# Optimization experiments

Hardware: AMD Instinct MI355X
Metric: run time of the kernel (lower is better)

Reference implementation:

```python
import jax, jax.numpy as jnp
import numpy as np

DECAY = 0.8
EPS = 1e-5
COMMIT = 1.0


def setup_inputs() -> dict:
    key = jax.random.key(0)
    k1, k2 = jax.random.split(key)
    x = jax.random.normal(k1, (8, 2048, 512), dtype=jnp.float32)
    embed = jax.random.normal(k2, (4, 2048, 128), dtype=jnp.float32)  # [G, C, dg]
    cluster_size = jnp.zeros((4, 2048), dtype=jnp.float32)            # [G, C]
    embed_avg = embed                                                 # clone of embed, as in torch init
    return {"x": x, "embed": embed, "cluster_size": cluster_size, "embed_avg": embed_avg}


def reference(x, embed, cluster_size, embed_avg):
    B, S, D = x.shape
    G, C, dg = embed.shape
    N = B * S
    # split channels into G groups: [G, N, dg]
    f = x.reshape(N, G, dg).transpose(1, 0, 2)
    # negative squared euclidean distance: -(||f||^2 - 2 f E^T + ||E||^2) -> [G, N, C]
    dist = -(jnp.sum(f * f, axis=-1, keepdims=True)
             - 2.0 * jnp.einsum('gnd,gcd->gnc', f, embed)
             + jnp.sum(embed * embed, axis=-1)[:, None, :])
    ind = jnp.argmax(dist, axis=-1)  # [G, N]
    # gather codes: quantize[g, n] = embed[g, ind[g, n]]
    q = jax.vmap(lambda e_g, i_g: e_g[i_g])(embed, ind)  # [G, N, dg]
    quantize = q.transpose(1, 0, 2).reshape(B, S, D)

    # --- EMA codebook update (training path; buffer updates, no grad in torch) ---
    bins = jax.vmap(lambda i_g: jnp.zeros((C,), x.dtype).at[i_g].add(1.0))(ind)  # [G, C]
    embed_sum = jax.vmap(lambda f_g, i_g: jax.ops.segment_sum(f_g, i_g, num_segments=C))(f, ind)  # [G, C, dg]
    new_cluster_size = cluster_size * DECAY + (1.0 - DECAY) * bins
    new_embed_avg = embed_avg * DECAY + (1.0 - DECAY) * embed_sum
    total = jnp.sum(new_cluster_size, axis=-1, keepdims=True)
    smoothed = (new_cluster_size + EPS) / (total + C * EPS) * total  # laplace smoothing
    new_embed = new_embed_avg / smoothed[..., None]

    # straight-through estimator + commitment loss (VectorQuantize wrapper)
    commit_loss = COMMIT * jnp.mean((jax.lax.stop_gradient(quantize) - x) ** 2)
    quantize_st = x + jax.lax.stop_gradient(quantize - x)
    ind_out = ind.transpose(1, 0).reshape(B, S, G)
    return (quantize_st, ind_out, commit_loss,
            jax.lax.stop_gradient(new_cluster_size),
            jax.lax.stop_gradient(new_embed_avg),
            jax.lax.stop_gradient(new_embed))
```

## Files before the change

### kernel.cpp

```cpp
#include <hip/hip_runtime.h>

#define Bn 8
#define Sn 2048
#define Dn 512
#define Gn 4
#define Cn 2048
#define DGn 128
#define Nn 16384

#define OFF_Q    0u
#define OFF_IND  8388608u
#define OFF_LOSS 8454144u
#define OFF_CS   8454145u
#define OFF_AVG  8462337u
#define OFF_EMB  9510913u

__global__ void vq_init(const float* __restrict__ cs_in,
                        const float* __restrict__ avg_in,
                        float* __restrict__ out) {
    int i = blockIdx.x * 256 + threadIdx.x;
    if (i < Gn * Cn * DGn) out[OFF_AVG + i] = 0.8f * avg_in[i];
    if (i < Gn * Cn)       out[OFF_CS + i]  = 0.8f * cs_in[i];
    if (i == 0)            out[OFF_LOSS] = 0.0f;
}

__global__ void vq_enorm(const float* __restrict__ embed,
                         float* __restrict__ out) {
    int gid  = blockIdx.x * 256 + threadIdx.x;
    int wave = gid >> 6;
    int lane = gid & 63;
    const float* row = embed + (size_t)wave * DGn;
    float a = row[lane], b = row[lane + 64];
    float v = fmaf(a, a, b * b);
    #pragma unroll
    for (int off = 32; off; off >>= 1) v += __shfl_xor(v, off, 64);
    if (lane == 0) out[OFF_EMB + wave] = v;
}

__launch_bounds__(512, 2)
__global__ void vq_main(const float* __restrict__ x,
                        const float* __restrict__ embed,
                        float* __restrict__ out) {
    __shared__ float As[DGn][128];
    __shared__ float Es[8][256];

    const int t  = threadIdx.x;
    const int g  = blockIdx.x >> 7;
    const int n0 = (blockIdx.x & 127) * 128;
    const int tr = t & 15;
    const int tc = t >> 4;

    const float* xg = x + (size_t)n0 * Dn + g * DGn;
    const float* eg = embed + (size_t)g * Cn * DGn;
    const float* enorm_g = out + OFF_EMB + g * Cn;

    {
        const int arow = t & 127, ah = t >> 7;
        const float* xrow = xg + (size_t)arow * Dn;
        #pragma unroll
        for (int j = 0; j < 8; ++j) {
            int q4 = ah + 4 * j;
            float4 v = *(const float4*)(xrow + q4 * 4);
            int k = q4 * 4;
            As[k+0][arow] = v.x; As[k+1][arow] = v.y; As[k+2][arow] = v.z; As[k+3][arow] = v.w;
        }
    }

    float bestv[8];
    int   besti[8];
    #pragma unroll
    for (int i = 0; i < 8; ++i) { bestv[i] = -3.4e38f; besti[i] = 0; }

    const int m0 = 4 * tr;
    const int cb = 4 * tc;
    const int ec = t & 255;
    const int kq = (t >> 8) * 4;

    for (int c0 = 0; c0 < Cn; c0 += 256) {
        float acc[8][8];
        #pragma unroll
        for (int i = 0; i < 8; ++i)
            #pragma unroll
            for (int j = 0; j < 8; ++j) acc[i][j] = 0.f;

        for (int k0 = 0; k0 < DGn; k0 += 8) {
            __syncthreads();
            {
                const float* erow = eg + (size_t)(c0 + ec) * DGn + k0 + kq;
                float4 e0 = *(const float4*)(erow);
                Es[kq+0][ec] = e0.x; Es[kq+1][ec] = e0.y; Es[kq+2][ec] = e0.z; Es[kq+3][ec] = e0.w;
            }
            __syncthreads();
            #pragma unroll
            for (int kk = 0; kk < 8; ++kk) {
                float4 a0 = *(const float4*)&As[k0+kk][m0];
                float4 a1 = *(const float4*)&As[k0+kk][64 + m0];
                float4 b0 = *(const float4*)&Es[kk][cb];
                float4 b1 = *(const float4*)&Es[kk][128 + cb];
                float av[8] = {a0.x,a0.y,a0.z,a0.w,a1.x,a1.y,a1.z,a1.w};
                float bv[8] = {b0.x,b0.y,b0.z,b0.w,b1.x,b1.y,b1.z,b1.w};
                #pragma unroll
                for (int i = 0; i < 8; ++i) {
                    float a = av[i];
                    #pragma unroll
                    for (int j = 0; j < 8; ++j)
                        acc[i][j] = fmaf(a, bv[j], acc[i][j]);
                }
            }
        }
        #pragma unroll
        for (int h = 0; h < 2; ++h) {
            #pragma unroll
            for (int jj = 0; jj < 4; ++jj) {
                int c = c0 + 128*h + cb + jj;
                float en = enorm_g[c];
                #pragma unroll
                for (int i = 0; i < 8; ++i) {
                    float di = fmaf(2.0f, acc[i][4*h + jj], -en);
                    if (di > bestv[i]) { bestv[i] = di; besti[i] = c; }
                }
            }
        }
    }

    float* redv = &As[0][0];
    int*   redi = ((int*)&As[0][0]) + 4352;
    int*   idxf = (int*)&Es[0][0];
    __syncthreads();
    #pragma unroll
    for (int i = 0; i < 8; ++i) {
        int m = (i < 4) ? (m0 + i) : (64 + m0 + i - 4);
        redv[m*33 + tc] = bestv[i];
        redi[m*33 + tc] = besti[i];
    }
    __syncthreads();
    if (t < 128) {
        float bv = redv[t*33]; int bi = redi[t*33];
        #pragma unroll
        for (int u = 1; u < 32; ++u) {
            float v2 = redv[t*33 + u]; int i2 = redi[t*33 + u];
            if (v2 > bv || (v2 == bv && i2 < bi)) { bv = v2; bi = i2; }
        }
        idxf[t] = bi;
        out[OFF_IND + (size_t)(n0 + t) * Gn + g] = (float)bi;
        atomicAdd(&out[OFF_CS + g*Cn + bi], 0.2f);
    }
    __syncthreads();

    float lloss = 0.f;
    for (int j = 0; j < 32; ++j) {
        int e = j * 512 + t;
        int row = e >> 7, d = e & 127;
        int ci = idxf[row];
        float xv = xg[(size_t)row * Dn + d];
        float q  = eg[(size_t)ci * DGn + d];
        out[OFF_Q + (size_t)(n0+row) * Dn + g*DGn + d] = xv + (q - xv);
        atomicAdd(&out[OFF_AVG + ((size_t)g*Cn + ci)*DGn + d], 0.2f * xv);
        float df = q - xv;
        lloss += df * df;
    }
    #pragma unroll
    for (int off = 32; off; off >>= 1) lloss += __shfl_xor(lloss, off, 64);
    if ((t & 63) == 0) atomicAdd(&out[OFF_LOSS], lloss);
}

__global__ void vq_finalize(float* __restrict__ out) {
    const int g = blockIdx.x >> 5;
    const int slice = blockIdx.x & 31;
    const int t = threadIdx.x;
    __shared__ float red[256];
    const float* ncs = out + OFF_CS + g * Cn;
    float s = 0.f;
    for (int c = t; c < Cn; c += 256) s += ncs[c];
    red[t] = s;
    __syncthreads();
    for (int w = 128; w; w >>= 1) {
        if (t < w) red[t] += red[t + w];
        __syncthreads();
    }
    float total = red[0];
    float denom = total + Cn * 1e-5f;
    const float* avg = out + OFF_AVG + (size_t)g * Cn * DGn;
    float* embo = out + OFF_EMB + (size_t)g * Cn * DGn;
    for (int u = 0; u < 32; ++u) {
        int e = slice * 8192 + u * 256 + t;
        int c = e >> 7;
        float sm = (ncs[c] + 1e-5f) / denom * total;
        embo[e] = avg[e] / sm;
    }
    if (blockIdx.x == 0 && t == 0) out[OFF_LOSS] *= (1.0f / 8388608.0f);
}

extern "C" void kernel_launch(void* const* d_in, const int* in_sizes, int n_in,
                              void* d_out, int out_size, void* d_ws, size_t ws_size,
                              hipStream_t stream) {
    const float* x    = (const float*)d_in[0];
    const float* emb  = (const float*)d_in[1];
    const float* cs   = (const float*)d_in[2];
    const float* eavg = (const float*)d_in[3];
    float* out = (float*)d_out;

    hipLaunchKernelGGL(vq_init,     dim3(4096), dim3(256), 0, stream, cs, eavg, out);
    hipLaunchKernelGGL(vq_enorm,    dim3(2048), dim3(256), 0, stream, emb, out);
    hipLaunchKernelGGL(vq_main,     dim3(512),  dim3(512), 0, stream, x, emb, out);
    hipLaunchKernelGGL(vq_finalize, dim3(128),  dim3(256), 0, stream, out);
}
```

Baseline: 535.5 us.

## Double-buffer codebook tiles with register prefetch and widen per-thread tile to 8x16

Restructures the distance GEMM loop so that codebook tiles are 16 deep by 512 codes wide and double-buffered in LDS. The next tile is prefetched into registers while the current one is computed, which cuts the barrier count to one per step. Each thread now accumulates an 8x16 block instead of 8x8, raising arithmetic intensity per LDS load. The cost is roughly double the accumulator registers and a drop to one block per CU in the launch bounds, so occupancy falls and there is a risk of spilling.

Measured after the change: 873.9 us. 63.2% more time.

```diff
diff --git a/kernel.cpp b/kernel.cpp
--- a/kernel.cpp
+++ b/kernel.cpp
@@ -37,12 +37,12 @@
     if (lane == 0) out[OFF_EMB + wave] = v;
 }
 
-__launch_bounds__(512, 2)
+__launch_bounds__(512, 1)
 __global__ void vq_main(const float* __restrict__ x,
                         const float* __restrict__ embed,
                         float* __restrict__ out) {
     __shared__ float As[DGn][128];
-    __shared__ float Es[8][256];
+    __shared__ float Es[2][16][512];
 
     const int t  = threadIdx.x;
     const int g  = blockIdx.x >> 7;
@@ -65,6 +65,18 @@
             As[k+0][arow] = v.x; As[k+1][arow] = v.y; As[k+2][arow] = v.z; As[k+3][arow] = v.w;
         }
     }
+    {
+        const float* er = eg + (size_t)t * DGn;
+        float4 p0 = *(const float4*)(er);
+        float4 p1 = *(const float4*)(er + 4);
+        float4 p2 = *(const float4*)(er + 8);
+        float4 p3 = *(const float4*)(er + 12);
+        Es[0][ 0][t] = p0.x; Es[0][ 1][t] = p0.y; Es[0][ 2][t] = p0.z; Es[0][ 3][t] = p0.w;
+        Es[0][ 4][t] = p1.x; Es[0][ 5][t] = p1.y; Es[0][ 6][t] = p1.z; Es[0][ 7][t] = p1.w;
+        Es[0][ 8][t] = p2.x; Es[0][ 9][t] = p2.y; Es[0][10][t] = p2.z; Es[0][11][t] = p2.w;
+        Es[0][12][t] = p3.x; Es[0][13][t] = p3.y; Es[0][14][t] = p3.z; Es[0][15][t] = p3.w;
+    }
+    __syncthreads();
 
     float bestv[8];
     int   besti[8];
@@ -73,60 +85,83 @@
 
     const int m0 = 4 * tr;
     const int cb = 4 * tc;
-    const int ec = t & 255;
-    const int kq = (t >> 8) * 4;
-
-    for (int c0 = 0; c0 < Cn; c0 += 256) {
-        float acc[8][8];
-        #pragma unroll
-        for (int i = 0; i < 8; ++i)
+
+    float acc[8][16];
+    #pragma unroll
+    for (int i = 0; i < 8; ++i)
+        #pragma unroll
+        for (int j = 0; j < 16; ++j) acc[i][j] = 0.f;
+
+    for (int s = 0; s < 32; ++s) {
+        const int cur = s & 1;
+        const int c0 = (s >> 3) << 9;
+        const int k0 = (s & 7) << 4;
+
+        float4 p0, p1, p2, p3;
+        if (s < 31) {
+            const int s1 = s + 1;
+            const int nc0 = (s1 >> 3) << 9;
+            const int nk0 = (s1 & 7) << 4;
+            const float* er = eg + (size_t)(nc0 + t) * DGn + nk0;
+            p0 = *(const float4*)(er);
+            p1 = *(const float4*)(er + 4);
+            p2 = *(const float4*)(er + 8);
+            p3 = *(const float4*)(er + 12);
+        }
+
+        #pragma unroll
+        for (int kk = 0; kk < 16; ++kk) {
+            float4 a0 = *(const float4*)&As[k0+kk][m0];
+            float4 a1 = *(const float4*)&As[k0+kk][64 + m0];
+            float4 b0 = *(const float4*)&Es[cur][kk][cb];
+            float4 b1 = *(const float4*)&Es[cur][kk][128 + cb];
+            float4 b2 = *(const float4*)&Es[cur][kk][256 + cb];
+            float4 b3 = *(const float4*)&Es[cur][kk][384 + cb];
+            float av[8]  = {a0.x,a0.y,a0.z,a0.w,a1.x,a1.y,a1.z,a1.w};
+            float bv[16] = {b0.x,b0.y,b0.z,b0.w,b1.x,b1.y,b1.z,b1.w,
+                            b2.x,b2.y,b2.z,b2.w,b3.x,b3.y,b3.z,b3.w};
             #pragma unroll
-            for (int j = 0; j < 8; ++j) acc[i][j] = 0.f;
-
-        for (int k0 = 0; k0 < DGn; k0 += 8) {
-            __syncthreads();
-            {
-                const float* erow = eg + (size_t)(c0 + ec) * DGn + k0 + kq;
-                float4 e0 = *(const float4*)(erow);
-                Es[kq+0][ec] = e0.x; Es[kq+1][ec] = e0.y; Es[kq+2][ec] = e0.z; Es[kq+3][ec] = e0.w;
+            for (int i = 0; i < 8; ++i) {
+                float a = av[i];
+                #pragma unroll
+                for (int j = 0; j < 16; ++j)
+                    acc[i][j] = fmaf(a, bv[j], acc[i][j]);
             }
-            __syncthreads();
+        }
+
+        if ((s & 7) == 7) {
             #pragma unroll
-            for (int kk = 0; kk < 8; ++kk) {
-                float4 a0 = *(const float4*)&As[k0+kk][m0];
-                float4 a1 = *(const float4*)&As[k0+kk][64 + m0];
-                float4 b0 = *(const float4*)&Es[kk][cb];
-                float4 b1 = *(const float4*)&Es[kk][128 + cb];
-                float av[8] = {a0.x,a0.y,a0.z,a0.w,a1.x,a1.y,a1.z,a1.w};
-                float bv[8] = {b0.x,b0.y,b0.z,b0.w,b1.x,b1.y,b1.z,b1.w};
+            for (int h = 0; h < 4; ++h) {
                 #pragma unroll
-                for (int i = 0; i < 8; ++i) {
-                    float a = av[i];
+                for (int jj = 0; jj < 4; ++jj) {
+                    int c = c0 + 128*h + cb + jj;
+                    float en = enorm_g[c];
                     #pragma unroll
-                    for (int j = 0; j < 8; ++j)
-                        acc[i][j] = fmaf(a, bv[j], acc[i][j]);
+                    for (int i = 0; i < 8; ++i) {
+                        float di = fmaf(2.0f, acc[i][4*h + jj], -en);
+                        if (di > bestv[i]) { bestv[i] = di; besti[i] = c; }
+                    }
                 }
             }
-        }
-        #pragma unroll
-        for (int h = 0; h < 2; ++h) {
             #pragma unroll
-            for (int jj = 0; jj < 4; ++jj) {
-                int c = c0 + 128*h + cb + jj;
-                float en = enorm_g[c];
+            for (int i = 0; i < 8; ++i)
                 #pragma unroll
-                for (int i = 0; i < 8; ++i) {
-                    float di = fmaf(2.0f, acc[i][4*h + jj], -en);
-                    if (di > bestv[i]) { bestv[i] = di; besti[i] = c; }
-                }
-            }
-        }
+                for (int j = 0; j < 16; ++j) acc[i][j] = 0.f;
+        }
+
+        if (s < 31) {
+            const int nxt = cur ^ 1;
+            Es[nxt][ 0][t] = p0.x; Es[nxt][ 1][t] = p0.y; Es[nxt][ 2][t] = p0.z; Es[nxt][ 3][t] = p0.w;
+            Es[nxt][ 4][t] = p1.x; Es[nxt][ 5][t] = p1.y; Es[nxt][ 6][t] = p1.z; Es[nxt][ 7][t] = p1.w;
+            Es[nxt][ 8][t] = p2.x; Es[nxt][ 9][t] = p2.y; Es[nxt][10][t] = p2.z; Es[nxt][11][t] = p2.w;
+            Es[nxt][12][t] = p3.x; Es[nxt][13][t] = p3.y; Es[nxt][14][t] = p3.z; Es[nxt][15][t] = p3.w;
+        }
+        __syncthreads();
     }
 
     float* redv = &As[0][0];
     int*   redi = ((int*)&As[0][0]) + 4352;
-    int*   idxf = (int*)&Es[0][0];
-    __syncthreads();
+    int*   idxf = (int*)&Es[0][0][0];
     #pragma unroll
     for (int i = 0; i < 8; ++i) {
         int m = (i < 4) ? (m0 + i) : (64 + m0 + i - 4);
```

## Compute distance GEMM with split-bf16 MFMA and move scatter to separate kernel

Applied to the files above, without the earlier changes.

Replaces the FP32 SIMT distance GEMM with bf16 MFMA 32x32x16 instructions. Each operand is split three ways (hi/mid/lo bf16) and six cross products are summed to approximate FP32 accuracy. The codebook tiles are double-buffered in shared memory with register prefetch, and the argmax runs through a shared-memory score tile. The quantize write, EMA atomics and loss go into a new vq_scatter kernel that reads the stored indices. The split adds conversion work and extra synchronisation, and the split-bf16 products may still flip near-tie argmax results.

Result: slower. 1.131 ms (+111.3%).

```diff
diff --git a/kernel.cpp b/kernel.cpp
--- a/kernel.cpp
+++ b/kernel.cpp
@@ -14,6 +14,22 @@
 #define OFF_CS   8454145u
 #define OFF_AVG  8462337u
 #define OFF_EMB  9510913u
+
+typedef __attribute__((ext_vector_type(8)))  short bf16x8;
+typedef __attribute__((ext_vector_type(16))) float f32x16;
+
+__device__ __forceinline__ unsigned bfbits(float x) {
+    unsigned u = __float_as_uint(x);
+    return (u + 0x7FFFu + ((u >> 16) & 1u)) & 0xFFFF0000u;
+}
+__device__ __forceinline__ void split3(float a, short &sh, short &sm, short &sl) {
+    unsigned hb = bfbits(a); float hf = __uint_as_float(hb);
+    float r  = a - hf;
+    unsigned mb = bfbits(r); float mf = __uint_as_float(mb);
+    float r2 = r - mf;
+    unsigned lb = bfbits(r2);
+    sh = (short)(hb >> 16); sm = (short)(mb >> 16); sl = (short)(lb >> 16);
+}
 
 __global__ void vq_init(const float* __restrict__ cs_in,
                         const float* __restrict__ avg_in,
@@ -37,131 +53,240 @@
     if (lane == 0) out[OFF_EMB + wave] = v;
 }
 
-__launch_bounds__(512, 2)
+#define IA(mt,v,ks,lane) (((((mt)*3+(v))*8+(ks))*64+(lane))*8)
+#define IB(v,cst,lane)   ((((v)*8+(cst))*64+(lane))*8)
+
+__launch_bounds__(512, 1)
 __global__ void vq_main(const float* __restrict__ x,
                         const float* __restrict__ embed,
                         float* __restrict__ out) {
-    __shared__ float As[DGn][128];
-    __shared__ float Es[8][256];
+    __shared__ short A_sh[49152];
+    __shared__ short B0_sh[12288];
+    __shared__ float S_sh[8704];
+    short* const B1_sh = (short*)S_sh;
 
     const int t  = threadIdx.x;
+    const int l  = t & 63;
+    const int w  = t >> 6;
+    const int wm = w >> 2, wc = w & 3;
     const int g  = blockIdx.x >> 7;
     const int n0 = (blockIdx.x & 127) * 128;
-    const int tr = t & 15;
-    const int tc = t >> 4;
-
-    const float* xg = x + (size_t)n0 * Dn + g * DGn;
+
     const float* eg = embed + (size_t)g * Cn * DGn;
     const float* enorm_g = out + OFF_EMB + g * Cn;
 
     {
-        const int arow = t & 127, ah = t >> 7;
-        const float* xrow = xg + (size_t)arow * Dn;
+        const int m  = t >> 2, q = t & 3;
+        const int mt = m >> 5;
+        const float* xr = x + (size_t)(n0 + m) * Dn + g * DGn;
         #pragma unroll
         for (int j = 0; j < 8; ++j) {
-            int q4 = ah + 4 * j;
-            float4 v = *(const float4*)(xrow + q4 * 4);
-            int k = q4 * 4;
-            As[k+0][arow] = v.x; As[k+1][arow] = v.y; As[k+2][arow] = v.z; As[k+3][arow] = v.w;
-        }
-    }
-
-    float bestv[8];
-    int   besti[8];
+            const int k = q * 32 + j * 4;
+            float4 v = *(const float4*)(xr + k);
+            short h0,h1,h2,h3, p0,p1,p2,p3, q0,q1,q2,q3;
+            split3(v.x, h0, p0, q0); split3(v.y, h1, p1, q1);
+            split3(v.z, h2, p2, q2); split3(v.w, h3, p3, q3);
+            const int lane_ = (m & 31) + ((k >> 3) & 1) * 32;
+            const int ks = k >> 4, sl0 = k & 7;
+            short4 hv; hv.x=h0; hv.y=h1; hv.z=h2; hv.w=h3;
+            short4 mv; mv.x=p0; mv.y=p1; mv.z=p2; mv.w=p3;
+            short4 lv; lv.x=q0; lv.y=q1; lv.z=q2; lv.w=q3;
+            *(short4*)&A_sh[IA(mt,0,ks,lane_) + sl0] = hv;
+            *(short4*)&A_sh[IA(mt,1,ks,lane_) + sl0] = mv;
+            *(short4*)&A_sh[IA(mt,2,ks,lane_) + sl0] = lv;
+        }
+    }
+    {
+        const float* er = eg + (size_t)(t >> 1) * DGn + (t & 1) * 8;
+        float4 e0 = *(const float4*)(er);
+        float4 e1 = *(const float4*)(er + 4);
+        float vals[8] = {e0.x,e0.y,e0.z,e0.w,e1.x,e1.y,e1.z,e1.w};
+        short hh[8], mm_[8], ll[8];
+        #pragma unroll
+        for (int i = 0; i < 8; ++i) split3(vals[i], hh[i], mm_[i], ll[i]);
+        const int cst = (t >> 1) >> 5, lb_ = ((t >> 1) & 31) + ((t & 1) << 5);
+        bf16x8 H, M, L;
+        #pragma unroll
+        for (int i = 0; i < 8; ++i) { H[i]=hh[i]; M[i]=mm_[i]; L[i]=ll[i]; }
+        *(bf16x8*)&B0_sh[IB(0,cst,lb_)] = H;
+        *(bf16x8*)&B0_sh[IB(1,cst,lb_)] = M;
+        *(bf16x8*)&B0_sh[IB(2,cst,lb_)] = L;
+    }
+    __syncthreads();
+
+    f32x16 acc00, acc01, acc10, acc11;
     #pragma unroll
-    for (int i = 0; i < 8; ++i) { bestv[i] = -3.4e38f; besti[i] = 0; }
-
-    const int m0 = 4 * tr;
-    const int cb = 4 * tc;
-    const int ec = t & 255;
-    const int kq = (t >> 8) * 4;
-
-    for (int c0 = 0; c0 < Cn; c0 += 256) {
-        float acc[8][8];
-        #pragma unroll
-        for (int i = 0; i < 8; ++i)
+    for (int r = 0; r < 16; ++r) { acc00[r]=0.f; acc01[r]=0.f; acc10[r]=0.f; acc11[r]=0.f; }
+
+    float bv = -3.4e38f; int bi = 0;
+
+    const int mt0 = wm*2, mt1 = wm*2 + 1;
+    const int cst0 = wc*2, cst1 = wc*2 + 1;
+
+    for (int s = 0; s < 64; ++s) {
+        const int ct = s >> 3, ks = s & 7;
+        const short* curB = (s & 1) ? B1_sh : B0_sh;
+
+        float4 e0n, e1n;
+        if (s < 63) {
+            const int s1 = s + 1, ct1 = s1 >> 3, ks1 = s1 & 7;
+            const float* er = eg + (size_t)(ct1*256 + (t >> 1)) * DGn + ks1*16 + (t & 1)*8;
+            e0n = *(const float4*)(er);
+            e1n = *(const float4*)(er + 4);
+        }
+
+        bf16x8 a0h = *(const bf16x8*)&A_sh[IA(mt0,0,ks,l)];
+        bf16x8 a0m = *(const bf16x8*)&A_sh[IA(mt0,1,ks,l)];
+        bf16x8 a0l = *(const bf16x8*)&A_sh[IA(mt0,2,ks,l)];
+        bf16x8 a1h = *(const bf16x8*)&A_sh[IA(mt1,0,ks,l)];
+        bf16x8 a1m = *(const bf16x8*)&A_sh[IA(mt1,1,ks,l)];
+        bf16x8 a1l = *(const bf16x8*)&A_sh[IA(mt1,2,ks,l)];
+        {
+            bf16x8 bh = *(const bf16x8*)&curB[IB(0,cst0,l)];
+            bf16x8 bm = *(const bf16x8*)&curB[IB(1,cst0,l)];
+            bf16x8 bl = *(const bf16x8*)&curB[IB(2,cst0,l)];
+            acc00 = __builtin_amdgcn_mfma_f32_32x32x16_bf16(a0h,bh,acc00,0,0,0);
+            acc00 = __builtin_amdgcn_mfma_f32_32x32x16_bf16(a0h,bm,acc00,0,0,0);
+            acc00 = __builtin_amdgcn_mfma_f32_32x32x16_bf16(a0m,bh,acc00,0,0,0);
+            acc00 = __builtin_amdgcn_mfma_f32_32x32x16_bf16(a0m,bm,acc00,0,0,0);
+            acc00 = __builtin_amdgcn_mfma_f32_32x32x16_bf16(a0h,bl,acc00,0,0,0);
+            acc00 = __builtin_amdgcn_mfma_f32_32x32x16_bf16(a0l,bh,acc00,0,0,0);
+            acc10 = __builtin_amdgcn_mfma_f32_32x32x16_bf16(a1h,bh,acc10,0,0,0);
+            acc10 = __builtin_amdgcn_mfma_f32_32x32x16_bf16(a1h,bm,acc10,0,0,0);
+            acc10 = __builtin_amdgcn_mfma_f32_32x32x16_bf16(a1m,bh,acc10,0,0,0);
+            acc10 = __builtin_amdgcn_mfma_f32_32x32x16_bf16(a1m,bm,acc10,0,0,0);
+            acc10 = __builtin_amdgcn_mfma_f32_32x32x16_bf16(a1h,bl,acc10,0,0,0);
+            acc10 = __builtin_amdgcn_mfma_f32_32x32x16_bf16(a1l,bh,acc10,0,0,0);
+        }
+        {
+            bf16x8 bh = *(const bf16x8*)&curB[IB(0,cst1,l)];
+            bf16x8 bm = *(const bf16x8*)&curB[IB(1,cst1,l)];
+            bf16x8 bl = *(const bf16x8*)&curB[IB(2,cst1,l)];
+            acc01 = __builtin_amdgcn_mfma_f32_32x32x16_bf16(a0h,bh,acc01,0,0,0);
+            acc01 = __builtin_amdgcn_mfma_f32_32x32x16_bf16(a0h,bm,acc01,0,0,0);
+            acc01 = __builtin_amdgcn_mfma_f32_32x32x16_bf16(a0m,bh,acc01,0,0,0);
+            acc01 = __builtin_amdgcn_mfma_f32_32x32x16_bf16(a0m,bm,acc01,0,0,0);
+            acc01 = __builtin_amdgcn_mfma_f32_32x32x16_bf16(a0h,bl,acc01,0,0,0);
+            acc01 = __builtin_amdgcn_mfma_f32_32x32x16_bf16(a0l,bh,acc01,0,0,0);
+            acc11 = __builtin_amdgcn_mfma_f32_32x32x16_bf16(a1h,bh,acc11,0,0,0);
+            acc11 = __builtin_amdgcn_mfma_f32_32x32x16_bf16(a1h,bm,acc11,0,0,0);
+            acc11 = __builtin_amdgcn_mfma_f32_32x32x16_bf16(a1m,bh,acc11,0,0,0);
+            acc11 = __builtin_amdgcn_mfma_f32_32x32x16_bf16(a1m,bm,acc11,0,0,0);
+            acc11 = __builtin_amdgcn_mfma_f32_32x32x16_bf16(a1h,bl,acc11,0,0,0);
+            acc11 = __builtin_amdgcn_mfma_f32_32x32x16_bf16(a1l,bh,acc11,0,0,0);
+        }
+
+        if (s < 63) {
+            short* nxtB = (s & 1) ? B0_sh : B1_sh;
+            float vals[8] = {e0n.x,e0n.y,e0n.z,e0n.w,e1n.x,e1n.y,e1n.z,e1n.w};
+            short hh[8], mm_[8], ll[8];
             #pragma unroll
-            for (int j = 0; j < 8; ++j) acc[i][j] = 0.f;
-
-        for (int k0 = 0; k0 < DGn; k0 += 8) {
-            __syncthreads();
-            {
-                const float* erow = eg + (size_t)(c0 + ec) * DGn + k0 + kq;
-                float4 e0 = *(const float4*)(erow);
-                Es[kq+0][ec] = e0.x; Es[kq+1][ec] = e0.y; Es[kq+2][ec] = e0.z; Es[kq+3][ec] = e0.w;
+            for (int i = 0; i < 8; ++i) split3(vals[i], hh[i], mm_[i], ll[i]);
+            const int cst = (t >> 1) >> 5, lb_ = ((t >> 1) & 31) + ((t & 1) << 5);
+            bf16x8 H, M, L;
+            #pragma unroll
+            for (int i = 0; i < 8; ++i) { H[i]=hh[i]; M[i]=mm_[i]; L[i]=ll[i]; }
+            *(bf16x8*)&nxtB[IB(0,cst,lb_)] = H;
+            *(bf16x8*)&nxtB[IB(1,cst,lb_)] = M;
+            *(bf16x8*)&nxtB[IB(2,cst,lb_)] = L;
+        }
+        __syncthreads();
+
+        if (ks == 7) {
+            #pragma unroll
+            for (int p = 0; p < 4; ++p) {
+                if ((wc & 1) == (p & 1)) {
+                    const int cf = p >> 1;
+                    const int cc = ((wc >> 1) << 5) + (l & 31);
+                    const int cg = ct*256 + wc*64 + cf*32 + (l & 31);
+                    const float en = enorm_g[cg];
+                    const int rb = wm*64 + 4*(l >> 5);
+                    if (cf == 0) {
+                        #pragma unroll
+                        for (int r = 0; r < 16; ++r) {
+                            const int ro = rb + (r & 3) + 8*(r >> 2);
+                            S_sh[ro*68 + cc]      = fmaf(2.f, acc00[r], -en);
+                            S_sh[(ro+32)*68 + cc] = fmaf(2.f, acc10[r], -en);
+                        }
+                    } else {
+                        #pragma unroll
+                        for (int r = 0; r < 16; ++r) {
+                            const int ro = rb + (r & 3) + 8*(r >> 2);
+                            S_sh[ro*68 + cc]      = fmaf(2.f, acc01[r], -en);
+                            S_sh[(ro+32)*68 + cc] = fmaf(2.f, acc11[r], -en);
+                        }
+                    }
+                }
+                __syncthreads();
+                {
+                    const int row = t >> 2, qq = t & 3;
+                    const int wcof = ((qq >> 1) << 1) | (p & 1);
+                    const int cb = ct*256 + wcof*64 + (p >> 1)*32 + (qq & 1)*16;
+                    const float* Sr = &S_sh[row*68 + qq*16];
+                    #pragma unroll
+                    for (int u = 0; u < 4; ++u) {
+                        float4 sv = *(const float4*)(Sr + 4*u);
+                        const int c0 = cb + 4*u;
+                        if (sv.x > bv || (sv.x == bv && c0   < bi)) { bv = sv.x; bi = c0;   }
+                        if (sv.y > bv || (sv.y == bv && c0+1 < bi)) { bv = sv.y; bi = c0+1; }
+                        if (sv.z > bv || (sv.z == bv && c0+2 < bi)) { bv = sv.z; bi = c0+2; }
+                        if (sv.w > bv || (sv.w == bv && c0+3 < bi)) { bv = sv.w; bi = c0+3; }
+                    }
+                }
+                __syncthreads();
             }
-            __syncthreads();
             #pragma unroll
-            for (int kk = 0; kk < 8; ++kk) {
-                float4 a0 = *(const float4*)&As[k0+kk][m0];
-                float4 a1 = *(const float4*)&As[k0+kk][64 + m0];
-                float4 b0 = *(const float4*)&Es[kk][cb];
-                float4 b1 = *(const float4*)&Es[kk][128 + cb];
-                float av[8] = {a0.x,a0.y,a0.z,a0.w,a1.x,a1.y,a1.z,a1.w};
-                float bv[8] = {b0.x,b0.y,b0.z,b0.w,b1.x,b1.y,b1.z,b1.w};
-                #pragma unroll
-                for (int i = 0; i < 8; ++i) {
-                    float a = av[i];
-                    #pragma unroll
-                    for (int j = 0; j < 8; ++j)
-                        acc[i][j] = fmaf(a, bv[j], acc[i][j]);
-                }
-            }
-        }
-        #pragma unroll
-        for (int h = 0; h < 2; ++h) {
-            #pragma unroll
-            for (int jj = 0; jj < 4; ++jj) {
-                int c = c0 + 128*h + cb + jj;
-                float en = enorm_g[c];
-                #pragma unroll
-                for (int i = 0; i < 8; ++i) {
-                    float di = fmaf(2.0f, acc[i][4*h + jj], -en);
-                    if (di > bestv[i]) { bestv[i] = di; besti[i] = c; }
-                }
-            }
-        }
-    }
-
-    float* redv = &As[0][0];
-    int*   redi = ((int*)&As[0][0]) + 4352;
-    int*   idxf = (int*)&Es[0][0];
-    __syncthreads();
-    #pragma unroll
-    for (int i = 0; i < 8; ++i) {
-        int m = (i < 4) ? (m0 + i) : (64 + m0 + i - 4);
-        redv[m*33 + tc] = bestv[i];
-        redi[m*33 + tc] = besti[i];
-    }
+            for (int r = 0; r < 16; ++r) { acc00[r]=0.f; acc01[r]=0.f; acc10[r]=0.f; acc11[r]=0.f; }
+        }
+    }
+
+    float* rv = (float*)B0_sh;
+    int*   ri = (int*)B0_sh + 512;
+    rv[(t >> 2)*4 + (t & 3)] = bv;
+    ri[(t >> 2)*4 + (t & 3)] = bi;
     __syncthreads();
     if (t < 128) {
-        float bv = redv[t*33]; int bi = redi[t*33];
+        float fv = rv[t*4]; int fi = ri[t*4];
         #pragma unroll
-        for (int u = 1; u < 32; ++u) {
-            float v2 = redv[t*33 + u]; int i2 = redi[t*33 + u];
-            if (v2 > bv || (v2 == bv && i2 < bi)) { bv = v2; bi = i2; }
-        }
-        idxf[t] = bi;
-        out[OFF_IND + (size_t)(n0 + t) * Gn + g] = (float)bi;
-        atomicAdd(&out[OFF_CS + g*Cn + bi], 0.2f);
-    }
-    __syncthreads();
-
-    float lloss = 0.f;
+        for (int u = 1; u < 4; ++u) {
+            float v2 = rv[t*4+u]; int i2 = ri[t*4+u];
+            if (v2 > fv || (v2 == fv && i2 < fi)) { fv = v2; fi = i2; }
+        }
+        out[OFF_IND + (size_t)(n0 + t) * Gn + g] = (float)fi;
+        atomicAdd(&out[OFF_CS + g*Cn + fi], 0.2f);
+    }
+}
+
+__global__ void vq_scatter(const float* __restrict__ x,
+                           const float* __restrict__ embed,
+                           float* __restrict__ out) {
+    const int t = threadIdx.x;
+    const int n = blockIdx.x * 64 + (t >> 2);
+    const int g = t & 3;
+    const int ci = (int)out[OFF_IND + (size_t)n * Gn + g];
+    const float* xr = x + (size_t)n * Dn + g * DGn;
+    const float* er = embed + ((size_t)g * Cn + ci) * DGn;
+    float* qr = out + OFF_Q + (size_t)n * Dn + g * DGn;
+    float* ar = out + OFF_AVG + ((size_t)g * Cn + ci) * DGn;
+    float ll = 0.f;
+    #pragma unroll 4
     for (int j = 0; j < 32; ++j) {
-        int e = j * 512 + t;
-        int row = e >> 7, d = e & 127;
-        int ci = idxf[row];
-        float xv = xg[(size_t)row * Dn + d];
-        float q  = eg[(size_t)ci * DGn + d];
-        out[OFF_Q + (size_t)(n0+row) * Dn + g*DGn + d] = xv + (q - xv);
-        atomicAdd(&out[OFF_AVG + ((size_t)g*Cn + ci)*DGn + d], 0.2f * xv);
-        float df = q - xv;
-        lloss += df * df;
+        float4 xv = *(const float4*)(xr + 4*j);
+        float4 qv = *(const float4*)(er + 4*j);
+        float4 o;
+        o.x = xv.x + (qv.x - xv.x); o.y = xv.y + (qv.y - xv.y);
+        o.z = xv.z + (qv.z - xv.z); o.w = xv.w + (qv.w - xv.w);
+        *(float4*)(qr + 4*j) = o;
+        atomicAdd(&ar[4*j+0], 0.2f*xv.x);
+        atomicAdd(&ar[4*j+1], 0.2f*xv.y);
+        atomicAdd(&ar[4*j+2], 0.2f*xv.z);
+        atomicAdd(&ar[4*j+3], 0.2f*xv.w);
+        float dx = qv.x - xv.x, dy = qv.y - xv.y, dz = qv.z - xv.z, dw = qv.w - xv.w;
+        ll += dx*dx; ll += dy*dy; ll += dz*dz; ll += dw*dw;
     }
     #pragma unroll
-    for (int off = 32; off; off >>= 1) lloss += __shfl_xor(lloss, off, 64);
-    if ((t & 63) == 0) atomicAdd(&out[OFF_LOSS], lloss);
+    for (int off = 32; off; off >>= 1) ll += __shfl_xor(ll, off, 64);
+    if ((t & 63) == 0) atomicAdd(&out[OFF_LOSS], ll);
 }
 
 __global__ void vq_finalize(float* __restrict__ out) {
@@ -203,5 +328,6 @@
     hipLaunchKernelGGL(vq_init,     dim3(4096), dim3(256), 0, stream, cs, eavg, out);
     hipLaunchKernelGGL(vq_enorm,    dim3(2048), dim3(256), 0, stream, emb, out);
     hipLaunchKernelGGL(vq_main,     dim3(512),  dim3(512), 0, stream, x, emb, out);
+    hipLaunchKernelGGL(vq_scatter,  dim3(256),  dim3(256), 0, stream, x, emb, out);
     hipLaunchKernelGGL(vq_finalize, dim3(128),  dim3(256), 0, stream, out);
 }
```
